# Performance work log

Measured on AMD Instinct MI355X. Metric: run time of the kernel, lower is better.

The kernel has to match this reference:

```python
import jax, jax.numpy as jnp
import numpy as np

D_MODEL = 1024
N_HEADS = 16
D_K = D_MODEL // N_HEADS
D_FF = 4096
EPS = 1e-5


def _layer_norm(x, gamma, beta):
    mu = jnp.mean(x, axis=-1, keepdims=True)
    var = jnp.var(x, axis=-1, keepdims=True)
    return (x - mu) * jax.lax.rsqrt(var + EPS) * gamma + beta


def setup_inputs() -> dict:
    key = jax.random.key(0)
    ks = jax.random.split(key, 16)
    s = 1.0 / np.sqrt(D_MODEL)
    sf = 1.0 / np.sqrt(D_FF)
    return {
        "x": jax.random.normal(ks[0], (2, 2048, D_MODEL), dtype=jnp.float32),
        "Wq": jax.random.uniform(ks[1], (D_MODEL, D_MODEL), minval=-s, maxval=s),
        "bq": jax.random.uniform(ks[2], (D_MODEL,), minval=-s, maxval=s),
        "Wk": jax.random.uniform(ks[3], (D_MODEL, D_MODEL), minval=-s, maxval=s),
        "bk": jax.random.uniform(ks[4], (D_MODEL,), minval=-s, maxval=s),
        "Wv": jax.random.uniform(ks[5], (D_MODEL, D_MODEL), minval=-s, maxval=s),
        "bv": jax.random.uniform(ks[6], (D_MODEL,), minval=-s, maxval=s),
        "Wo": jax.random.uniform(ks[7], (D_MODEL, D_MODEL), minval=-s, maxval=s),
        "bo": jax.random.uniform(ks[8], (D_MODEL,), minval=-s, maxval=s),
        "W1": jax.random.uniform(ks[9], (D_MODEL, D_FF), minval=-s, maxval=s),
        "b1": jax.random.uniform(ks[10], (D_FF,), minval=-s, maxval=s),
        "W2": jax.random.uniform(ks[11], (D_FF, D_MODEL), minval=-sf, maxval=sf),
        "b2": jax.random.uniform(ks[12], (D_MODEL,), minval=-sf, maxval=sf),
        "g1": jnp.ones((D_MODEL,)),
        "be1": jnp.zeros((D_MODEL,)),
        "g2": jnp.ones((D_MODEL,)),
        "be2": jnp.zeros((D_MODEL,)),
    }


def reference(x, Wq, bq, Wk, bk, Wv, bv, Wo, bo, W1, b1, W2, b2, g1, be1, g2, be2):
    B, S, _ = x.shape

    def heads(y):  # (B,S,D) -> (B,H,S,dk)
        return y.reshape(B, S, N_HEADS, D_K).transpose(0, 2, 1, 3)

    q = heads(x @ Wq + bq)
    k = heads(x @ Wk + bk)
    v = heads(x @ Wv + bv)

    scores = jnp.einsum("bhqd,bhkd->bhqk", q, k) / np.sqrt(D_K)
    attn = jax.nn.softmax(scores, axis=-1)
    out = jnp.einsum("bhqk,bhkd->bhqd", attn, v)
    out = out.transpose(0, 2, 1, 3).reshape(B, S, D_MODEL)
    attn_out = out @ Wo + bo

    resid_mid = _layer_norm(x + attn_out, g1, be1)
    ff = jnp.maximum(resid_mid @ W1 + b1, 0.0) @ W2 + b2
    return _layer_norm(resid_mid + ff, g2, be2)
```

## Files before the change

### kernel.cpp

```cpp
#include <hip/hip_runtime.h>

#define DM   1024
#define DFF  4096
#define NH   16
#define DKH  64
#define SEQ  2048
#define BATCH 2
#define ROWS (BATCH*SEQ)
#define QKS  2048

typedef __bf16 bf16x8 __attribute__((ext_vector_type(8)));
typedef float  f32x4  __attribute__((ext_vector_type(4)));

__device__ __forceinline__ unsigned short f2b(float f) {
    unsigned int u = __builtin_bit_cast(unsigned int, f);
    u += 0x7fffu + ((u >> 16) & 1u);
    return (unsigned short)(u >> 16);
}
__device__ __forceinline__ float b2f(unsigned short u) {
    return __builtin_bit_cast(float, (unsigned int)u << 16);
}

__device__ __forceinline__ void gl_lds16(const unsigned short* g, unsigned short* l) {
    __builtin_amdgcn_global_load_lds(
        (const __attribute__((address_space(1))) unsigned int*)(const void*)g,
        (__attribute__((address_space(3))) unsigned int*)(void*)l, 16, 0, 0);
}

__global__ __launch_bounds__(256) void k_f32_to_bf16(const float* __restrict__ in,
                                                     unsigned short* __restrict__ out, int n4) {
    int i = blockIdx.x * 256 + threadIdx.x;
    if (i < n4) {
        float4 v = ((const float4*)in)[i];
        ushort4 u;
        u.x = f2b(v.x); u.y = f2b(v.y); u.z = f2b(v.z); u.w = f2b(v.w);
        ((ushort4*)out)[i] = u;
    }
}

__global__ __launch_bounds__(256) void k_transpose_bf16(const float* __restrict__ W,
                                                        unsigned short* __restrict__ WT,
                                                        int R, int C) {
    __shared__ float t[32][33];
    int c0 = blockIdx.x * 32, r0 = blockIdx.y * 32;
    int tx = threadIdx.x, ty = threadIdx.y;
#pragma unroll
    for (int i = 0; i < 4; i++) {
        int r = ty + i * 8;
        t[r][tx] = W[(size_t)(r0 + r) * C + c0 + tx];
    }
    __syncthreads();
#pragma unroll
    for (int i = 0; i < 4; i++) {
        int r = ty + i * 8;
        WT[(size_t)(c0 + r) * R + r0 + tx] = f2b(t[tx][r]);
    }
}

template<int WM, int WN, bool OUTF32, bool RELU, bool BIASROW, bool VPERM, bool SCALE2>
__global__ __launch_bounds__(256) void k_gemm_bt(const unsigned short* __restrict__ A,
                                                 const unsigned short* __restrict__ BT,
                                                 const float* __restrict__ bias,
                                                 const float* __restrict__ bias2,
                                                 int bsplit, float sc2,
                                                 void* __restrict__ Cout,
                                                 int M, int N, int K) {
    constexpr int BM = 2 * WM, BN = 2 * WN;
    constexpr int MT = WM / 16, NT = WN / 16;
    constexpr int IA = BM / 32, IB = BN / 32;
    __shared__ unsigned short As[BM][64] __attribute__((aligned(16)));
    __shared__ unsigned short Bs[BN][64] __attribute__((aligned(16)));
    int tid = threadIdx.x;
    int w = tid >> 6, l = tid & 63;
    int wr = w >> 1, wc = w & 1;
    int l15 = l & 15, lg = l >> 4;

    int bid = blockIdx.y * gridDim.x + blockIdx.x;
    int nwg = gridDim.x * gridDim.y;
    int swz = (bid & 7) * (nwg >> 3) + (bid >> 3);
    int m0 = (swz / gridDim.x) * BM, n0 = (swz % gridDim.x) * BN;

    int lr8 = l >> 3;
    int gsrc = (l & 7) ^ lr8;
    const unsigned short* Abase = A  + (size_t)(m0 + w * (BM / 4) + lr8) * K + gsrc * 8;
    const unsigned short* Bbase = BT + (size_t)(n0 + w * (BN / 4) + lr8) * K + gsrc * 8;

    f32x4 acc[MT][NT] = {};

    int nk = K >> 6;
    for (int kt = 0; kt < nk; ++kt) {
        __syncthreads();
#pragma unroll
        for (int it = 0; it < IA; ++it)
            gl_lds16(Abase + (size_t)(it * 8) * K + kt * 64, &As[w * (BM / 4) + it * 8][0]);
#pragma unroll
        for (int it = 0; it < IB; ++it)
            gl_lds16(Bbase + (size_t)(it * 8) * K + kt * 64, &Bs[w * (BN / 4) + it * 8][0]);
        __syncthreads();
#pragma unroll
        for (int ks = 0; ks < 2; ++ks) {
            int glog = ks * 4 + lg;
            bf16x8 af[MT], bfr[NT];
#pragma unroll
            for (int mt = 0; mt < MT; ++mt) {
                int row = wr * WM + mt * 16 + l15;
                af[mt] = *(const bf16x8*)&As[row][(glog ^ (row & 7)) << 3];
            }
#pragma unroll
            for (int nt = 0; nt < NT; ++nt) {
                int row = wc * WN + nt * 16 + l15;
                bfr[nt] = *(const bf16x8*)&Bs[row][(glog ^ (row & 7)) << 3];
            }
#pragma unroll
            for (int mt = 0; mt < MT; ++mt)
#pragma unroll
                for (int nt = 0; nt < NT; ++nt)
                    acc[mt][nt] = __builtin_amdgcn_mfma_f32_16x16x32_bf16(af[mt], bfr[nt], acc[mt][nt], 0, 0, 0);
        }
    }
    float browv[MT][4];
    if (BIASROW) {
#pragma unroll
        for (int mt = 0; mt < MT; ++mt)
#pragma unroll
            for (int r = 0; r < 4; ++r)
                browv[mt][r] = bias[m0 + wr * WM + mt * 16 + lg * 4 + r];
    }
#pragma unroll
    for (int nt = 0; nt < NT; ++nt) {
        int colo = VPERM ? (32 * (nt >> 1) + 4 * (nt & 1) + 8 * (l15 >> 2) + (l15 & 3))
                         : (nt * 16 + l15);
        int col = n0 + wc * WN + colo;
        float bv = BIASROW ? 0.f : (col < bsplit ? bias[col] : bias2[col - bsplit]);
#pragma unroll
        for (int mt = 0; mt < MT; ++mt) {
#pragma unroll
            for (int r = 0; r < 4; ++r) {
                int row = m0 + wr * WM + mt * 16 + lg * 4 + r;
                float v = acc[mt][nt][r] + (BIASROW ? browv[mt][r] : bv);
                if (SCALE2 && col >= bsplit) v *= sc2;
                if (RELU) v = fmaxf(v, 0.f);
                if (OUTF32) ((float*)Cout)[(size_t)row * N + col] = v;
                else        ((unsigned short*)Cout)[(size_t)row * N + col] = f2b(v);
            }
        }
    }
}

__global__ __launch_bounds__(512) void k_attn(const unsigned short* __restrict__ Q,
                                              const unsigned short* __restrict__ Kb,
                                              const unsigned short* __restrict__ VT,
                                              unsigned short* __restrict__ O) {
    __shared__ unsigned short ksA[64][64] __attribute__((aligned(16)));
    __shared__ unsigned short vsA[64][64] __attribute__((aligned(16)));
    __shared__ unsigned short ksB[64][64] __attribute__((aligned(16)));
    __shared__ unsigned short vsB[64][64] __attribute__((aligned(16)));

    int tid = threadIdx.x;
    int w = tid >> 6, l = tid & 63;
    int l15 = l & 15, lg = l >> 4;

    int bid = blockIdx.y * gridDim.x + blockIdx.x;
    int bh = (bid & 7) * 4 + ((bid >> 3) & 3);
    int qt = bid >> 5;
    int b = bh >> 4, h = bh & 15;
    int row0 = qt * 128;

    const unsigned short* qg  = Q  + (size_t)b * SEQ * QKS + h * DKH;
    const unsigned short* kg  = Kb + (size_t)b * SEQ * QKS + h * DKH;
    const unsigned short* vtg = VT + (size_t)(h * DKH) * ROWS + (size_t)b * SEQ;

    int lr8 = l >> 3;
    int gsrc = (l & 7) ^ lr8;

    const unsigned short* kp0 = kg  + (size_t)(w * 8 + lr8) * QKS + gsrc * 8;
    const unsigned short* vp0 = vtg + (size_t)(w * 8 + lr8) * ROWS + gsrc * 8;

    gl_lds16(kp0, &ksA[w * 8][0]);
    gl_lds16(vp0, &vsA[w * 8][0]);
    kp0 += (size_t)64 * QKS; vp0 += 64;

    bf16x8 aq[2];
    {
        int qrow = row0 + w * 16 + l15;
        aq[0] = *(const bf16x8*)(qg + (size_t)qrow * QKS + lg * 8);
        aq[1] = *(const bf16x8*)(qg + (size_t)qrow * QKS + (4 + lg) * 8);
    }

    int dsoff[2][4];
#pragma unroll
    for (int ksi = 0; ksi < 2; ksi++)
#pragma unroll
        for (int nt = 0; nt < 4; nt++) {
            int row = nt * 16 + l15;
            int glog = ksi * 4 + lg;
            dsoff[ksi][nt] = row * 128 + ((glog ^ (row & 7)) << 4);
        }

    union { bf16x8 v; unsigned int u[4]; } ones;
#pragma unroll
    for (int i = 0; i < 4; i++) ones.u[i] = 0x3f803f80u;

    f32x4 o[4] = {};
    f32x4 osum = {};

    __syncthreads();

    auto body = [&](unsigned short (&kbuf)[64][64], unsigned short (&vbuf)[64][64],
                    unsigned short (&knext)[64][64], unsigned short (&vnext)[64][64],
                    bool doStage) {
        if (doStage) {
            gl_lds16(kp0, &knext[w * 8][0]);
            gl_lds16(vp0, &vnext[w * 8][0]);
            kp0 += (size_t)64 * QKS; vp0 += 64;
        }

        f32x4 s[4] = {};
        __builtin_amdgcn_s_setprio(1);
#pragma unroll
        for (int ksi = 0; ksi < 2; ksi++)
#pragma unroll
            for (int nt = 0; nt < 4; nt++) {
                bf16x8 bk = *(const bf16x8*)((const char*)&kbuf[0][0] + dsoff[ksi][nt]);
                s[nt] = __builtin_amdgcn_mfma_f32_16x16x32_bf16(bk, aq[ksi], s[nt], 0, 0, 0);
            }
        __builtin_amdgcn_s_setprio(0);

        union { bf16x8 v; unsigned int u[4]; } A0, A1;
#pragma unroll
        for (int nt = 0; nt < 4; nt++)
#pragma unroll
            for (int w2 = 0; w2 < 2; w2++) {
                float e0 = exp2f(s[nt][2 * w2]);
                float e1 = exp2f(s[nt][2 * w2 + 1]);
                unsigned int pk;
                asm("v_cvt_pk_bf16_f32 %0, %1, %2" : "=v"(pk) : "v"(e0), "v"(e1));
                if (nt < 2) A0.u[(nt & 1) * 2 + w2] = pk;
                else        A1.u[(nt & 1) * 2 + w2] = pk;
            }

        __builtin_amdgcn_s_setprio(1);
        osum = __builtin_amdgcn_mfma_f32_16x16x32_bf16(A0.v, ones.v, osum, 0, 0, 0);
        osum = __builtin_amdgcn_mfma_f32_16x16x32_bf16(A1.v, ones.v, osum, 0, 0, 0);
#pragma unroll
        for (int ksi = 0; ksi < 2; ksi++)
#pragma unroll
            for (int nt = 0; nt < 4; nt++) {
                bf16x8 bv = *(const bf16x8*)((const char*)&vbuf[0][0] + dsoff[ksi][nt]);
                o[nt] = __builtin_amdgcn_mfma_f32_16x16x32_bf16(ksi == 0 ? A0.v : A1.v, bv, o[nt], 0, 0, 0);
            }
        __builtin_amdgcn_s_setprio(0);

        __syncthreads();
    };

    for (int kt2 = 0; kt2 < 16; ++kt2) {
        body(ksA, vsA, ksB, vsB, true);
        body(ksB, vsB, ksA, vsA, kt2 < 15);
    }

    float rinv[4];
#pragma unroll
    for (int r = 0; r < 4; r++) rinv[r] = 1.f / osum[r];

    unsigned short* og = O + (size_t)b * SEQ * DM + h * DKH;
#pragma unroll
    for (int nt = 0; nt < 4; nt++) {
        int d = nt * 16 + l15;
#pragma unroll
        for (int r = 0; r < 4; r++) {
            int srow_ = row0 + w * 16 + lg * 4 + r;
            og[(size_t)srow_ * DM + d] = f2b(o[nt][r] * rinv[r]);
        }
    }
}

template<bool WB16>
__global__ __launch_bounds__(256) void k_add_ln(const float* __restrict__ a,
                                                const float* __restrict__ b,
                                                const float* __restrict__ gamma,
                                                const float* __restrict__ beta,
                                                float* __restrict__ outf,
                                                unsigned short* __restrict__ outb) {
    __shared__ float red[8];
    int row = blockIdx.x, tid = threadIdx.x;
    float4 va = ((const float4*)(a + (size_t)row * DM))[tid];
    float4 vb = ((const float4*)(b + (size_t)row * DM))[tid];
    float4 v;
    v.x = va.x + vb.x; v.y = va.y + vb.y; v.z = va.z + vb.z; v.w = va.w + vb.w;
    float s = v.x + v.y + v.z + v.w;
    float q = v.x * v.x + v.y * v.y + v.z * v.z + v.w * v.w;
#pragma unroll
    for (int m = 1; m < 64; m <<= 1) { s += __shfl_xor(s, m); q += __shfl_xor(q, m); }
    if ((tid & 63) == 0) { red[tid >> 6] = s; red[4 + (tid >> 6)] = q; }
    __syncthreads();
    float tot  = red[0] + red[1] + red[2] + red[3];
    float totq = red[4] + red[5] + red[6] + red[7];
    float mu = tot * (1.f / DM);
    float var = totq * (1.f / DM) - mu * mu;
    float rs = rsqrtf(var + 1e-5f);
    float4 g  = ((const float4*)gamma)[tid];
    float4 be = ((const float4*)beta)[tid];
    float4 y;
    y.x = (v.x - mu) * rs * g.x + be.x;
    y.y = (v.y - mu) * rs * g.y + be.y;
    y.z = (v.z - mu) * rs * g.z + be.z;
    y.w = (v.w - mu) * rs * g.w + be.w;
    ((float4*)(outf + (size_t)row * DM))[tid] = y;
    if (WB16) {
        ushort4 u;
        u.x = f2b(y.x); u.y = f2b(y.y); u.z = f2b(y.z); u.w = f2b(y.w);
        ((ushort4*)(outb + (size_t)row * DM))[tid] = u;
    }
}

extern "C" void kernel_launch(void* const* d_in, const int* in_sizes, int n_in,
                              void* d_out, int out_size, void* d_ws, size_t ws_size,
                              hipStream_t stream) {
    const float* x   = (const float*)d_in[0];
    const float* Wq  = (const float*)d_in[1];
    const float* bq  = (const float*)d_in[2];
    const float* Wk  = (const float*)d_in[3];
    const float* bk  = (const float*)d_in[4];
    const float* Wv  = (const float*)d_in[5];
    const float* bv  = (const float*)d_in[6];
    const float* Wo  = (const float*)d_in[7];
    const float* bo  = (const float*)d_in[8];
    const float* W1  = (const float*)d_in[9];
    const float* b1  = (const float*)d_in[10];
    const float* W2  = (const float*)d_in[11];
    const float* b2  = (const float*)d_in[12];
    const float* g1  = (const float*)d_in[13];
    const float* be1 = (const float*)d_in[14];
    const float* g2  = (const float*)d_in[15];
    const float* be2 = (const float*)d_in[16];

    char* ws = (char*)d_ws;
    const size_t MB = 1u << 20;
    unsigned short* xb    = (unsigned short*)(ws + 0);
    unsigned short* WqkT  = (unsigned short*)(ws + 8 * MB);
    unsigned short* WvT   = (unsigned short*)(ws + 12 * MB);
    unsigned short* WoT   = (unsigned short*)(ws + 14 * MB);
    unsigned short* W1T   = (unsigned short*)(ws + 16 * MB);
    unsigned short* W2T   = (unsigned short*)(ws + 24 * MB);
    unsigned short* qkb   = (unsigned short*)(ws + 32 * MB);
    unsigned short* vT    = (unsigned short*)(ws + 48 * MB);
    float*          scrf  = (float*)(ws + 56 * MB);
    float*          resid = (float*)(ws + 72 * MB);
    unsigned short* residb= (unsigned short*)(ws + 88 * MB);
    unsigned short* h1    = (unsigned short*)(ws + 96 * MB);

    dim3 blk(256);
    dim3 tb(32, 8);
    const int BIG = 1 << 30;
    const float SC = 0.125f * 1.44269504f;

    k_f32_to_bf16<<<(ROWS * DM / 4 + 255) / 256, blk, 0, stream>>>(x, xb, ROWS * DM / 4);
    k_transpose_bf16<<<dim3(DM / 32, DM / 32), tb, 0, stream>>>(Wq, WqkT, DM, DM);
    k_transpose_bf16<<<dim3(DM / 32, DM / 32), tb, 0, stream>>>(Wk, WqkT + (size_t)DM * DM, DM, DM);
    k_transpose_bf16<<<dim3(DM / 32, DM / 32), tb, 0, stream>>>(Wv, WvT, DM, DM);
    k_transpose_bf16<<<dim3(DM / 32, DM / 32), tb, 0, stream>>>(Wo, WoT, DM, DM);
    k_transpose_bf16<<<dim3(DFF / 32, DM / 32), tb, 0, stream>>>(W1, W1T, DM, DFF);
    k_transpose_bf16<<<dim3(DM / 32, DFF / 32), tb, 0, stream>>>(W2, W2T, DFF, DM);

    k_gemm_bt<32, 64, false, false, false, false, true><<<dim3(QKS / 128, ROWS / 64), blk, 0, stream>>>(
        xb, WqkT, bq, bk, DM, SC, qkb, ROWS, QKS, DM);
    k_gemm_bt<32, 64, false, false, true, true, false><<<dim3(ROWS / 128, DM / 64), blk, 0, stream>>>(
        WvT, xb, bv, bv, BIG, 1.f, vT, DM, ROWS, DM);

    k_attn<<<dim3(SEQ / 128, BATCH * NH), dim3(512), 0, stream>>>(qkb, qkb + DM, vT, xb);

    k_gemm_bt<32, 64, true, false, false, false, false><<<dim3(DM / 128, ROWS / 64), blk, 0, stream>>>(
        xb, WoT, bo, bo, BIG, 1.f, scrf, ROWS, DM, DM);
    k_add_ln<true><<<ROWS, blk, 0, stream>>>(x, scrf, g1, be1, resid, residb);

    k_gemm_bt<64, 64, false, true, false, false, false><<<dim3(DFF / 128, ROWS / 128), blk, 0, stream>>>(
        residb, W1T, b1, b1, BIG, 1.f, h1, ROWS, DFF, DM);
    k_gemm_bt<32, 64, true, false, false, false, false><<<dim3(DM / 128, ROWS / 64), blk, 0, stream>>>(
        h1, W2T, b2, b2, BIG, 1.f, scrf, ROWS, DM, DFF);
    k_add_ln<false><<<ROWS, blk, 0, stream>>>(resid, scrf, g2, be2, (float*)d_out, nullptr);
}
```

Measured before the change: 258.4 us.

## Double-buffer LDS tiles in bf16 GEMM to overlap global loads with MFMA

New measurement: 271.9 us. +5.2%, slower.

```diff
diff --git a/kernel.cpp b/kernel.cpp
--- a/kernel.cpp
+++ b/kernel.cpp
@@ -57,7 +57,7 @@
     }
 }
 
-template<int WM, int WN, bool OUTF32, bool RELU, bool BIASROW, bool VPERM, bool SCALE2>
+template<int WM, int WN, bool OUTF32, bool RELU, bool BIASROW, bool VPERM, bool SCALE2, bool DBUF>
 __global__ __launch_bounds__(256) void k_gemm_bt(const unsigned short* __restrict__ A,
                                                  const unsigned short* __restrict__ BT,
                                                  const float* __restrict__ bias,
@@ -68,8 +68,9 @@
     constexpr int BM = 2 * WM, BN = 2 * WN;
     constexpr int MT = WM / 16, NT = WN / 16;
     constexpr int IA = BM / 32, IB = BN / 32;
-    __shared__ unsigned short As[BM][64] __attribute__((aligned(16)));
-    __shared__ unsigned short Bs[BN][64] __attribute__((aligned(16)));
+    constexpr int NB = DBUF ? 2 : 1;
+    __shared__ unsigned short As[NB][BM][64] __attribute__((aligned(16)));
+    __shared__ unsigned short Bs[NB][BN][64] __attribute__((aligned(16)));
     int tid = threadIdx.x;
     int w = tid >> 6, l = tid & 63;
     int wr = w >> 1, wc = w & 1;
@@ -87,16 +88,15 @@
 
     f32x4 acc[MT][NT] = {};
 
-    int nk = K >> 6;
-    for (int kt = 0; kt < nk; ++kt) {
-        __syncthreads();
+    auto stage = [&](int kt, int buf) {
 #pragma unroll
         for (int it = 0; it < IA; ++it)
-            gl_lds16(Abase + (size_t)(it * 8) * K + kt * 64, &As[w * (BM / 4) + it * 8][0]);
+            gl_lds16(Abase + (size_t)(it * 8) * K + kt * 64, &As[buf][w * (BM / 4) + it * 8][0]);
 #pragma unroll
         for (int it = 0; it < IB; ++it)
-            gl_lds16(Bbase + (size_t)(it * 8) * K + kt * 64, &Bs[w * (BN / 4) + it * 8][0]);
-        __syncthreads();
+            gl_lds16(Bbase + (size_t)(it * 8) * K + kt * 64, &Bs[buf][w * (BN / 4) + it * 8][0]);
+    };
+    auto compute = [&](int buf) {
 #pragma unroll
         for (int ks = 0; ks < 2; ++ks) {
             int glog = ks * 4 + lg;
@@ -104,12 +104,12 @@
 #pragma unroll
             for (int mt = 0; mt < MT; ++mt) {
                 int row = wr * WM + mt * 16 + l15;
-                af[mt] = *(const bf16x8*)&As[row][(glog ^ (row & 7)) << 3];
+                af[mt] = *(const bf16x8*)&As[buf][row][(glog ^ (row & 7)) << 3];
             }
 #pragma unroll
             for (int nt = 0; nt < NT; ++nt) {
                 int row = wc * WN + nt * 16 + l15;
-                bfr[nt] = *(const bf16x8*)&Bs[row][(glog ^ (row & 7)) << 3];
+                bfr[nt] = *(const bf16x8*)&Bs[buf][row][(glog ^ (row & 7)) << 3];
             }
 #pragma unroll
             for (int mt = 0; mt < MT; ++mt)
@@ -117,7 +117,30 @@
                 for (int nt = 0; nt < NT; ++nt)
                     acc[mt][nt] = __builtin_amdgcn_mfma_f32_16x16x32_bf16(af[mt], bfr[nt], acc[mt][nt], 0, 0, 0);
         }
-    }
+    };
+
+    int nk = K >> 6;
+    if (DBUF) {
+        stage(0, 0);
+        __syncthreads();
+        int nk2 = nk >> 1;
+        for (int t = 0; t < nk2; ++t) {
+            stage(2 * t + 1, 1);
+            compute(0);
+            __syncthreads();
+            if (2 * t + 2 < nk) stage(2 * t + 2, 0);
+            compute(1);
+            __syncthreads();
+        }
+    } else {
+        for (int kt = 0; kt < nk; ++kt) {
+            __syncthreads();
+            stage(kt, 0);
+            __syncthreads();
+            compute(0);
+        }
+    }
+
     float browv[MT][4];
     if (BIASROW) {
 #pragma unroll
@@ -363,20 +386,20 @@
     k_transpose_bf16<<<dim3(DFF / 32, DM / 32), tb, 0, stream>>>(W1, W1T, DM, DFF);
     k_transpose_bf16<<<dim3(DM / 32, DFF / 32), tb, 0, stream>>>(W2, W2T, DFF, DM);
 
-    k_gemm_bt<32, 64, false, false, false, false, true><<<dim3(QKS / 128, ROWS / 64), blk, 0, stream>>>(
+    k_gemm_bt<32, 64, false, false, false, false, true, true><<<dim3(QKS / 128, ROWS / 64), blk, 0, stream>>>(
         xb, WqkT, bq, bk, DM, SC, qkb, ROWS, QKS, DM);
-    k_gemm_bt<32, 64, false, false, true, true, false><<<dim3(ROWS / 128, DM / 64), blk, 0, stream>>>(
+    k_gemm_bt<32, 64, false, false, true, true, false, true><<<dim3(ROWS / 128, DM / 64), blk, 0, stream>>>(
         WvT, xb, bv, bv, BIG, 1.f, vT, DM, ROWS, DM);
 
     k_attn<<<dim3(SEQ / 128, BATCH * NH), dim3(512), 0, stream>>>(qkb, qkb + DM, vT, xb);
 
-    k_gemm_bt<32, 64, true, false, false, false, false><<<dim3(DM / 128, ROWS / 64), blk, 0, stream>>>(
+    k_gemm_bt<32, 64, true, false, false, false, false, true><<<dim3(DM / 128, ROWS / 64), blk, 0, stream>>>(
         xb, WoT, bo, bo, BIG, 1.f, scrf, ROWS, DM, DM);
     k_add_ln<true><<<ROWS, blk, 0, stream>>>(x, scrf, g1, be1, resid, residb);
 
-    k_gemm_bt<64, 64, false, true, false, false, false><<<dim3(DFF / 128, ROWS / 128), blk, 0, stream>>>(
+    k_gemm_bt<64, 64, false, true, false, false, false, false><<<dim3(DFF / 128, ROWS / 128), blk, 0, stream>>>(
         residb, W1T, b1, b1, BIG, 1.f, h1, ROWS, DFF, DM);
-    k_gemm_bt<32, 64, true, false, false, false, false><<<dim3(DM / 128, ROWS / 64), blk, 0, stream>>>(
+    k_gemm_bt<32, 64, true, false, false, false, false, true><<<dim3(DM / 128, ROWS / 64), blk, 0, stream>>>(
         h1, W2T, b2, b2, BIG, 1.f, scrf, ROWS, DM, DFF);
     k_add_ln<false><<<ROWS, blk, 0, stream>>>(resid, scrf, g2, be2, (float*)d_out, nullptr);
 }
```
